# Optimization experiments

Measured on AMD Instinct MI355X. Metric: run time of the kernel, lower is better.

## Reference

```python
import jax, jax.numpy as jnp
import numpy as np

B, T, D, N, K, H = 2, 2048, 2048, 16, 8, 128
WINDOW = 1024
SOFT_CAP = 50.0
Q_SCALE = H ** -0.5  # query_pre_attn_scalar
ROPE_BASE = 10000
ROPE_SCALE = 1.0
K_MASK = -2.3819763e38


def apply_rope(x, positions, base_frequency=ROPE_BASE, scale_factor=ROPE_SCALE):
    # x: [B, T, n, H], positions: [B, T]
    head_dim = x.shape[-1]
    fraction = 2.0 * jnp.arange(head_dim // 2, dtype=jnp.float32) / head_dim
    timescale = base_frequency ** fraction  # [H/2]
    sin_inp = positions[..., None].astype(jnp.float32) / timescale  # [B,T,H/2]
    sin_inp = sin_inp[..., None, :] / scale_factor  # [B,T,1,H/2]
    sin, cos = jnp.sin(sin_inp), jnp.cos(sin_inp)
    x1, x2 = jnp.split(x, 2, axis=-1)
    out = jnp.concatenate([x1 * cos - x2 * sin, x2 * cos + x1 * sin], axis=-1)
    return out.astype(x.dtype)


def rms_norm(x, scale, eps=1e-6):
    var = jnp.mean(jnp.square(x.astype(jnp.float32)), axis=-1, keepdims=True)
    normed = x * jax.lax.rsqrt(var + eps)
    return (normed * (1.0 + scale)).astype(x.dtype)


def setup_inputs() -> dict:
    key = jax.random.key(0)
    ks = jax.random.split(key, 4)
    x = jax.random.normal(ks[0], (B, T, D), jnp.float32)
    segment_pos = jnp.tile(jnp.arange(T, dtype=jnp.int32)[None, :], (B, 1))
    attn_mask = jnp.tril(jnp.ones((T, T), dtype=bool))[None].repeat(B, axis=0)
    w_q = jax.random.normal(ks[1], (N, D, H), jnp.float32) * (D ** -0.5)
    w_kv = jax.random.normal(ks[2], (2, K, D, H), jnp.float32) * (D ** -0.5)
    w_o = jax.random.normal(ks[3], (N, H, D), jnp.float32) * ((N * H) ** -0.5)
    q_norm_scale = jnp.zeros((H,), jnp.float32)
    k_norm_scale = jnp.zeros((H,), jnp.float32)
    return dict(x=x, w_q=w_q, w_kv=w_kv, w_o=w_o,
                q_norm_scale=q_norm_scale, k_norm_scale=k_norm_scale,
                segment_pos=segment_pos, attn_mask=attn_mask)


def reference(x, w_q, w_kv, w_o, q_norm_scale, k_norm_scale, segment_pos, attn_mask):
    # projections
    q = jnp.einsum('BTD,NDH->BTNH', x, w_q)              # [B,T,N,H]
    kv = jnp.einsum('BSD,CKDH->CBSKH', x, w_kv)          # [2,B,S,K,H]
    k, v = kv[0], kv[1]
    # QK RMSNorm
    q = rms_norm(q, q_norm_scale)
    k = rms_norm(k, k_norm_scale)
    # RoPE + query scaling
    q = apply_rope(q, segment_pos) * Q_SCALE
    k = apply_rope(k, segment_pos)
    # GQA logits
    G = N // K
    qg = q.reshape(B, T, K, G, H)
    logits = jnp.einsum('BTKGH,BSKH->BTKGS', qg, k).reshape(B, T, N, T)
    # soft cap
    logits = jnp.tanh(logits / SOFT_CAP) * SOFT_CAP
    # sliding-window mask combined with causal attn_mask
    pos_q = segment_pos[:, :, None]
    pos_k = segment_pos[:, None, :]
    sliding = (pos_k > pos_q - WINDOW) & (pos_k < pos_q + WINDOW)
    mask = attn_mask & sliding                           # [B,T,S]
    padded = jnp.where(mask[:, :, None, :], logits, K_MASK)
    probs = jax.nn.softmax(padded, axis=-1).astype(k.dtype)
    # GQA weighted values
    enc = jnp.einsum('BTKGS,BSKH->BTKGH', probs.reshape(B, T, K, G, T), v)
    enc = enc.reshape(B, T, N, H)
    # split/concat of navigator vs scribe heads is an identity on output
    return jnp.einsum('BTNH,NHD->BTD', enc, w_o)
```

## Files before the change

### kernel.cpp

```cpp
#include <hip/hip_runtime.h>
#include <stdint.h>

typedef __attribute__((ext_vector_type(8))) short short8;
typedef __attribute__((ext_vector_type(4))) float f32x4;

#define B_ 2
#define T_ 2048
#define D_ 2048
#define N_ 16
#define KH_ 8
#define H_ 128
#define WINDOW_ 1024

__device__ __forceinline__ uint16_t f2bf(float f) {
  union { float f; uint32_t u; } a; a.f = f;
  uint32_t u = a.u;
  return (uint16_t)((u + 0x7FFFu + ((u >> 16) & 1u)) >> 16);
}

__device__ __forceinline__ void gl_lds16(const void* g, void* l) {
  __builtin_amdgcn_global_load_lds((const __attribute__((address_space(1))) void*)g,
                                   (__attribute__((address_space(3))) void*)l, 16, 0, 0);
}

__global__ __launch_bounds__(256) void k_f2b4(const float* __restrict__ src,
                                              uint16_t* __restrict__ dst, long n) {
  long i = ((long)blockIdx.x * 256 + threadIdx.x) * 4;
  if (i >= n) return;
  float4 v = *(const float4*)(src + i);
  uint64_t p = (uint64_t)f2bf(v.x) | ((uint64_t)f2bf(v.y) << 16) |
               ((uint64_t)f2bf(v.z) << 32) | ((uint64_t)f2bf(v.w) << 48);
  *(uint64_t*)(dst + i) = p;
}

__global__ __launch_bounds__(256)
void k_transpose_f2b(const float* __restrict__ src, uint16_t* __restrict__ dst,
                     int R, int C, int nb1, long sbs1, long sbs2, long dbs,
                     long src_off, int srs) {
  __shared__ float tile[32][33];
  int z = blockIdx.z;
  int b1 = z % nb1, b2 = z / nb1;
  const float* s = src + src_off + (long)b1 * sbs1 + (long)b2 * sbs2;
  uint16_t* d = dst + (long)z * dbs;
  int c0 = blockIdx.x * 32, r0 = blockIdx.y * 32;
  int x = threadIdx.x, y = threadIdx.y;
#pragma unroll
  for (int j = 0; j < 4; ++j)
    tile[y + j * 8][x] = s[(long)(r0 + y + j * 8) * srs + (c0 + x)];
  __syncthreads();
#pragma unroll
  for (int j = 0; j < 4; ++j)
    d[(long)(c0 + y + j * 8) * R + (r0 + x)] = f2bf(tile[x][y + j * 8]);
}

__global__ __launch_bounds__(256)
void k_transpose_v(const float* __restrict__ kvg, uint16_t* __restrict__ vbt) {
  __shared__ float tile[32][33];
  int z = blockIdx.z;
  int kh = z % KH_, b = z / KH_;
  const float* s = kvg + (long)b * T_ * 2048 + 1024 + kh * H_;
  uint16_t* d = vbt + (long)z * H_ * T_;
  int h0 = blockIdx.x * 32, s0 = blockIdx.y * 32;
  int x = threadIdx.x, y = threadIdx.y;
#pragma unroll
  for (int j = 0; j < 4; ++j)
    tile[y + j * 8][x] = s[(long)(s0 + y + j * 8) * 2048 + (h0 + x)];
  __syncthreads();
#pragma unroll
  for (int j = 0; j < 4; ++j) {
    int h = h0 + y + j * 8;
    int si = s0 + x;
    int ss = (si & ~63) | ((((si >> 3) & 7) ^ (h & 7)) << 3) | (si & 7);
    d[(long)h * T_ + ss] = f2bf(tile[x][y + j * 8]);
  }
}

__global__ __launch_bounds__(512, 2)
void k_gemm8(const uint16_t* __restrict__ A, const uint16_t* __restrict__ Bt,
             float* __restrict__ C0, float* __restrict__ C1, int nbx, int splitc) {
  __shared__ __align__(16) uint16_t Ls[2][2][2][128 * 64];
  int tid = threadIdx.x, lane = tid & 63, w = tid >> 6;
  int wm = w >> 2, wn = w & 3;
  int fr = lane & 15, fgrp = lane >> 4;
  int bid = blockIdx.x;
  int k2 = bid >> 3;
  long by = (bid & 7) * 2 + k2 / nbx;
  long bx = k2 % nbx;
  long row0 = by * 256, col0 = bx * 256;

  int trow = tid >> 3;
  int kse = (((tid & 7) * 16) ^ ((trow & 7) << 4)) >> 1;
  const uint16_t* aS[2] = { A + (row0 + trow) * 2048 + kse,
                            A + (row0 + 128 + trow) * 2048 + kse };
  const uint16_t* bS[2] = { Bt + (col0 + trow) * 2048 + kse,
                            Bt + (col0 + 128 + trow) * 2048 + kse };
  char* ldsbase = (char*)Ls + w * 1024;

  int kx[2] = { (fgrp * 16) ^ ((fr & 7) << 4), (64 + fgrp * 16) ^ ((fr & 7) << 4) };
  int aoffb = (wm * 64 + fr) * 128;
  int boffb = (wn * 32 + fr) * 128;
  const char* LA = (const char*)Ls;
  const char* LB = LA + 65536;

  f32x4 acc[2][2][4][2];
#pragma unroll
  for (int qm = 0; qm < 2; ++qm)
#pragma unroll
    for (int qn = 0; qn < 2; ++qn)
#pragma unroll
      for (int m = 0; m < 4; ++m)
#pragma unroll
        for (int n = 0; n < 2; ++n) acc[qm][qn][m][n] = (f32x4){0.f, 0.f, 0.f, 0.f};

#define STG(MAT, SLOT, HALF, KT) do {                                      \
    const uint16_t* _g = (MAT ? bS[HALF] : aS[HALF]) + (KT) * 64;          \
    char* _l = ldsbase + (MAT) * 65536 + (SLOT) * 32768 + (HALF) * 16384;  \
    gl_lds16(_g, _l);                                                      \
    gl_lds16(_g + 64 * 2048, _l + 8192);                                   \
  } while (0)

#define PH(SLOT, QM, QN, STMT, VM) do {                                               \
    short8 _a[4][2], _b[2][2];                                                        \
    _Pragma("unroll") for (int m = 0; m < 4; ++m) {                                   \
      _a[m][0] = *(const short8*)(LA + (SLOT)*32768 + (QM)*16384 + aoffb + m*2048 + kx[0]); \
      _a[m][1] = *(const short8*)(LA + (SLOT)*32768 + (QM)*16384 + aoffb + m*2048 + kx[1]); } \
    _Pragma("unroll") for (int n = 0; n < 2; ++n) {                                   \
      _b[n][0] = *(const short8*)(LB + (SLOT)*32768 + (QN)*16384 + boffb + n*2048 + kx[0]); \
      _b[n][1] = *(const short8*)(LB + (SLOT)*32768 + (QN)*16384 + boffb + n*2048 + kx[1]); } \
    STMT;                                                                             \
    __builtin_amdgcn_s_barrier();                                                     \
    asm volatile("s_waitcnt lgkmcnt(0)" ::: "memory");                                \
    __builtin_amdgcn_sched_barrier(0);                                                \
    __builtin_amdgcn_s_setprio(1);                                                    \
    _Pragma("unroll") for (int m = 0; m < 4; ++m)                                     \
      _Pragma("unroll") for (int n = 0; n < 2; ++n) {                                 \
        acc[QM][QN][m][n] = __builtin_amdgcn_mfma_f32_16x16x32_bf16(_a[m][0], _b[n][0], acc[QM][QN][m][n], 0, 0, 0); \
        acc[QM][QN][m][n] = __builtin_amdgcn_mfma_f32_16x16x32_bf16(_a[m][1], _b[n][1], acc[QM][QN][m][n], 0, 0, 0); } \
    __builtin_amdgcn_s_setprio(0);                                                    \
    if (VM) { asm volatile("s_waitcnt vmcnt(4)" ::: "memory");                        \
              __builtin_amdgcn_sched_barrier(0); }                                    \
    __builtin_amdgcn_s_barrier();                                                     \
    __builtin_amdgcn_sched_barrier(0);                                                \
  } while (0)

  STG(0, 0, 0, 0); STG(1, 0, 0, 0); STG(1, 0, 1, 0); STG(0, 0, 1, 0);
  STG(0, 1, 0, 1); STG(1, 1, 0, 1);
  asm volatile("s_waitcnt vmcnt(4)" ::: "memory");
  __builtin_amdgcn_sched_barrier(0);
  __builtin_amdgcn_s_barrier();

#pragma unroll 1
  for (int it = 0; it < 16; ++it) {
    int t1 = 2 * it + 1, t2 = (2 * it + 2) & 31, t3 = (2 * it + 3) & 31;
    PH(0, 0, 0, STG(1, 1, 1, t1), 0);
    PH(0, 0, 1, STG(0, 1, 1, t1), 0);
    PH(0, 1, 0, STG(0, 0, 0, t2), 0);
    PH(0, 1, 1, STG(1, 0, 0, t2), 1);
    PH(1, 0, 0, STG(1, 0, 1, t2), 0);
    PH(1, 0, 1, STG(0, 0, 1, t2), 0);
    PH(1, 1, 0, STG(0, 1, 0, t3), 0);
    PH(1, 1, 1, STG(1, 1, 0, t3), 1);
  }
#undef PH
#undef STG

  int og = fgrp * 4;
  bool hic = (col0 >= splitc);
  float* Cb = hic ? C1 : C0;
  long cb = col0 - (hic ? splitc : 0);
#pragma unroll
  for (int qm = 0; qm < 2; ++qm)
#pragma unroll
    for (int qn = 0; qn < 2; ++qn)
#pragma unroll
      for (int m = 0; m < 4; ++m)
#pragma unroll
        for (int n = 0; n < 2; ++n) {
          long r = row0 + qm * 128 + wm * 64 + m * 16 + og;
          long c = cb + qn * 128 + wn * 32 + n * 16 + fr;
          float* cp = Cb + r * 2048 + c;
#pragma unroll
          for (int i = 0; i < 4; ++i) cp[(long)i * 2048] = acc[qm][qn][m][n][i];
        }
}

__global__ __launch_bounds__(512, 2)
void k_gemm8n(const uint16_t* __restrict__ A, const uint16_t* __restrict__ Bt,
              float* __restrict__ C, int nbx) {
  __shared__ __align__(16) uint16_t LsA[2][2][128 * 64];
  __shared__ __align__(16) uint16_t LsB[2][128 * 64];
  int tid = threadIdx.x, lane = tid & 63, w = tid >> 6;
  int wm = w >> 2, wn = w & 3;
  int fr = lane & 15, fgrp = lane >> 4;
  int bid = blockIdx.x;
  int k2 = bid >> 3;
  long by = (bid & 7) * 2 + k2 / nbx;
  long bx = k2 % nbx;
  long row0 = by * 256, col0 = bx * 128;

  int trow = tid >> 3;
  int kse = (((tid & 7) * 16) ^ ((trow & 7) << 4)) >> 1;
  const uint16_t* aS[2] = { A + (row0 + trow) * 2048 + kse,
                            A + (row0 + 128 + trow) * 2048 + kse };
  const uint16_t* bS = Bt + (col0 + trow) * 2048 + kse;
  char* ldsA_w = (char*)LsA + w * 1024;
  char* ldsB_w = (char*)LsB + w * 1024;

  int kx[2] = { (fgrp * 16) ^ ((fr & 7) << 4), (64 + fgrp * 16) ^ ((fr & 7) << 4) };
  int aoffb = (wm * 64 + fr) * 128;
  int boffb = (wn * 32 + fr) * 128;
  const char* LA = (const char*)LsA;
  const char* LB = (const char*)LsB;

  f32x4 acc[2][4][2];
#pragma unroll
  for (int qm = 0; qm < 2; ++qm)
#pragma unroll
    for (int m = 0; m < 4; ++m)
#pragma unroll
      for (int n = 0; n < 2; ++n) acc[qm][m][n] = (f32x4){0.f, 0.f, 0.f, 0.f};

#define STGA(SLOT, HALF, KT) do {                                \
    const uint16_t* _g = aS[HALF] + (KT) * 64;                   \
    char* _l = ldsA_w + (SLOT) * 32768 + (HALF) * 16384;         \
    gl_lds16(_g, _l);                                            \
    gl_lds16(_g + 64 * 2048, _l + 8192);                         \
  } while (0)
#define STGB(SLOT, KT) do {                                      \
    const uint16_t* _g = bS + (KT) * 64;                         \
    char* _l = ldsB_w + (SLOT) * 16384;                          \
    gl_lds16(_g, _l);                                            \
    gl_lds16(_g + 64 * 2048, _l + 8192);                         \
  } while (0)

#define PHN(SLOT, QM, STMT, VM) do {                                                  \
    short8 _a[4][2], _b[2][2];                                                        \
    _Pragma("unroll") for (int m = 0; m < 4; ++m) {                                   \
      _a[m][0] = *(const short8*)(LA + (SLOT)*32768 + (QM)*16384 + aoffb + m*2048 + kx[0]); \
      _a[m][1] = *(const short8*)(LA + (SLOT)*32768 + (QM)*16384 + aoffb + m*2048 + kx[1]); } \
    _Pragma("unroll") for (int n = 0; n < 2; ++n) {                                   \
      _b[n][0] = *(const short8*)(LB + (SLOT)*16384 + boffb + n*2048 + kx[0]);        \
      _b[n][1] = *(const short8*)(LB + (SLOT)*16384 + boffb + n*2048 + kx[1]); }      \
    STMT;                                                                             \
    __builtin_amdgcn_s_barrier();                                                     \
    asm volatile("s_waitcnt lgkmcnt(0)" ::: "memory");                                \
    __builtin_amdgcn_sched_barrier(0);                                                \
    __builtin_amdgcn_s_setprio(1);                                                    \
    _Pragma("unroll") for (int m = 0; m < 4; ++m)                                     \
      _Pragma("unroll") for (int n = 0; n < 2; ++n) {                                 \
        acc[QM][m][n] = __builtin_amdgcn_mfma_f32_16x16x32_bf16(_a[m][0], _b[n][0], acc[QM][m][n], 0, 0, 0); \
        acc[QM][m][n] = __builtin_amdgcn_mfma_f32_16x16x32_bf16(_a[m][1], _b[n][1], acc[QM][m][n], 0, 0, 0); } \
    __builtin_amdgcn_s_setprio(0);                                                    \
    if (VM) { asm volatile("s_waitcnt vmcnt(2)" ::: "memory");                        \
              __builtin_amdgcn_sched_barrier(0); }                                    \
    __builtin_amdgcn_s_barrier();                                                     \
    __builtin_amdgcn_sched_barrier(0);                                                \
  } while (0)

  STGA(0, 0, 0); STGA(0, 1, 0); STGB(0, 0); STGA(1, 0, 1);
  asm volatile("s_waitcnt vmcnt(2)" ::: "memory");
  __builtin_amdgcn_sched_barrier(0);
  __builtin_amdgcn_s_barrier();

#pragma unroll 1
  for (int it = 0; it < 16; ++it) {
    int t1 = 2 * it + 1, t2 = (2 * it + 2) & 31, t3 = (2 * it + 3) & 31;
    PHN(0, 0, { STGA(1, 1, t1); STGB(1, t1); }, 0);
    PHN(0, 1, STGA(0, 0, t2), 1);
    PHN(1, 0, { STGA(0, 1, t2); STGB(0, t2); }, 0);
    PHN(1, 1, STGA(1, 0, t3), 1);
  }
#undef PHN
#undef STGA
#undef STGB

  int og = fgrp * 4;
#pragma unroll
  for (int qm = 0; qm < 2; ++qm)
#pragma unroll
    for (int m = 0; m < 4; ++m)
#pragma unroll
      for (int n = 0; n < 2; ++n) {
        long r = row0 + qm * 128 + wm * 64 + m * 16 + og;
        long c = col0 + wn * 32 + n * 16 + fr;
        float* cp = C + r * 2048 + c;
#pragma unroll
        for (int i = 0; i < 4; ++i) cp[(long)i * 2048] = acc[qm][m][n][i];
      }
}

__global__ __launch_bounds__(256)
void k_qpost(const float* __restrict__ qg, const float* __restrict__ qs,
             uint16_t* __restrict__ qb) {
  int gw = blockIdx.x * 4 + (threadIdx.x >> 6);
  int lane = threadIdx.x & 63;
  int bt = gw / N_;
  int t = bt % T_;
  const float* src = qg + (long)gw * H_;
  float x1 = src[lane], x2 = src[lane + 64];
  float ssq = x1 * x1 + x2 * x2;
#pragma unroll
  for (int off = 1; off < 64; off <<= 1) ssq += __shfl_xor(ssq, off);
  float inv = rsqrtf(ssq * (1.0f / 128.0f) + 1e-6f);
  float n1 = x1 * inv * (1.0f + qs[lane]);
  float n2 = x2 * inv * (1.0f + qs[lane + 64]);
  float ts = powf(10000.0f, (float)lane * (2.0f / 128.0f));
  float ang = (float)t / ts;
  float sn, cs;
  sincosf(ang, &sn, &cs);
  const float QSC = 0.08838834764831845f;
  uint16_t* dp = qb + (long)gw * H_;
  dp[lane] = f2bf((n1 * cs - n2 * sn) * QSC);
  dp[lane + 64] = f2bf((n2 * cs + n1 * sn) * QSC);
}

__global__ __launch_bounds__(256)
void k_kpost(const float* __restrict__ kvg, const float* __restrict__ ks,
             uint16_t* __restrict__ kb) {
  int gw = blockIdx.x * 4 + (threadIdx.x >> 6);
  int lane = threadIdx.x & 63;
  int kh = gw % KH_;
  int bt = gw / KH_;
  int t = bt % T_, b = bt / T_;
  const float* src = kvg + (long)bt * (KH_ * H_ * 2) + kh * H_;
  float x1 = src[lane], x2 = src[lane + 64];
  float ssq = x1 * x1 + x2 * x2;
#pragma unroll
  for (int off = 1; off < 64; off <<= 1) ssq += __shfl_xor(ssq, off);
  float inv = rsqrtf(ssq * (1.0f / 128.0f) + 1e-6f);
  float n1 = x1 * inv * (1.0f + ks[lane]);
  float n2 = x2 * inv * (1.0f + ks[lane + 64]);
  float ts = powf(10000.0f, (float)lane * (2.0f / 128.0f));
  float ang = (float)t / ts;
  float sn, cs;
  sincosf(ang, &sn, &cs);
  int sw = (t & 7) << 3;
  uint16_t* dp = kb + ((long)(b * KH_ + kh) * T_ + t) * H_;
  dp[lane ^ sw] = f2bf(n1 * cs - n2 * sn);
  dp[(lane + 64) ^ sw] = f2bf(n2 * cs + n1 * sn);
}

__global__ __launch_bounds__(256, 4)
void k_attn(const uint16_t* __restrict__ qb, const uint16_t* __restrict__ kb,
            const uint16_t* __restrict__ vbt, uint16_t* __restrict__ enc) {
  __shared__ uint16_t Ks[64 * 128];
  __shared__ uint16_t Vs[128 * 64];
  __shared__ uint16_t Pl[4][16 * 64];
  int tid = threadIdx.x, lane = tid & 63, w = tid >> 6;
  int nt = T_ / 64;
  int blk = blockIdx.x;
  int tq = nt - 1 - (blk >> 5);
  int bn = blk & 31;
  int n = bn % N_, b = bn / N_;
  int kh = n >> 1;
  int t0 = tq * 64;
  int tw = t0 + w * 16;
  int fr = lane & 15, fgrp = lane >> 4, fk = fgrp * 8;
  int sw3 = fr & 7;

  const uint16_t* qrow = qb + ((long)(b * T_ + tw + fr) * N_ + n) * H_;
  short8 aq[4];
#pragma unroll
  for (int kk = 0; kk < 4; ++kk) aq[kk] = *(const short8*)(qrow + kk * 32 + fk);

  float lrow[4];
  f32x4 o[8];
#pragma unroll
  for (int i = 0; i < 4; ++i) lrow[i] = 0.0f;
#pragma unroll
  for (int hf = 0; hf < 8; ++hf) o[hf] = (f32x4){0.f, 0.f, 0.f, 0.f};

  int s_begin = t0 - (WINDOW_ - 1);
  if (s_begin < 0) s_begin = 0;
  s_begin &= ~63;
  int s_endex = t0 + 64;

  const uint16_t* kbase = kb + (long)(b * KH_ + kh) * T_ * H_;
  const uint16_t* vbase = vbt + (long)(b * KH_ + kh) * H_ * T_;
  int krow_st = tid >> 4, kcol_st = (tid & 15) * 8;
  int vrow_st = tid >> 3, vcol_st = (tid & 7) * 8;
  char* ldsK = (char*)Ks + w * 1024;
  char* ldsV = (char*)Vs + w * 1024;
  uint16_t* Pw = Pl[w];

  for (int s0 = s_begin; s0 < s_endex; s0 += 64) {
    __syncthreads();
#pragma unroll
    for (int j = 0; j < 4; ++j) {
      gl_lds16(kbase + (long)(s0 + j * 16 + krow_st) * H_ + kcol_st, ldsK + j * 4096);
      gl_lds16(vbase + (long)(j * 32 + vrow_st) * T_ + s0 + vcol_st, ldsV + j * 4096);
    }
    __syncthreads();
    if (s0 > tw + 15 || s0 + 63 < tw - (WINDOW_ - 1)) continue;

    f32x4 sc[4];
#pragma unroll
    for (int kc = 0; kc < 4; ++kc) {
      f32x4 a = (f32x4){0.f, 0.f, 0.f, 0.f};
      const uint16_t* kr = Ks + (kc * 16 + fr) * 128;
#pragma unroll
      for (int kk = 0; kk < 4; ++kk) {
        short8 bk = *(const short8*)(kr + ((((kk << 2) | fgrp) ^ sw3) << 3));
        a = __builtin_amdgcn_mfma_f32_16x16x32_bf16(aq[kk], bk, a, 0, 0, 0);
      }
      sc[kc] = a;
    }

    bool full = (s0 + 63 <= tw) && (s0 >= tw + 16 - WINDOW_);
#define SMBODY(FULL)                                                              \
    _Pragma("unroll") for (int i = 0; i < 4; ++i) {                               \
      int r = fgrp * 4 + i;                                                       \
      int rsw = (r & 7) << 3;                                                     \
      int trowq = tw + r;                                                         \
      float ps = 0.f;                                                             \
      _Pragma("unroll") for (int kc = 0; kc < 4; ++kc) {                          \
        float v = sc[kc][i];                                                      \
        float xx = v * 0.02f;                                                     \
        xx = fminf(1.0f, fmaxf(-1.0f, xx));                                       \
        float u = xx * xx;                                                        \
        float tt = xx * fmaf(u, fmaf(u, fmaf(u, -0.053968254f, 0.13333334f),      \
                                     -0.33333334f), 1.0f);                        \
        float p = __expf(fmaf(tt, 50.0f, -20.0f));                                \
        if (!(FULL)) {                                                            \
          int s = s0 + kc * 16 + fr;                                              \
          bool ok = (s <= trowq) && (s > trowq - WINDOW_);                        \
          p = ok ? p : 0.0f;                                                      \
        }                                                                         \
        ps += p;                                                                  \
        Pw[r * 64 + ((kc * 16 + fr) ^ rsw)] = f2bf(p);                            \
      }                                                                           \
      lrow[i] += ps;                                                              \
    }
    if (full) { SMBODY(true) } else { SMBODY(false) }
#undef SMBODY

    short8 pa0 = *(const short8*)(Pw + fr * 64 + ((fgrp ^ sw3) << 3));
    short8 pa1 = *(const short8*)(Pw + fr * 64 + (((4 | fgrp) ^ sw3) << 3));
#pragma unroll
    for (int hf = 0; hf < 8; ++hf) {
      const uint16_t* vr = Vs + (hf * 16 + fr) * 64;
      short8 bv0 = *(const short8*)(vr + ((fgrp ^ sw3) << 3));
      short8 bv1 = *(const short8*)(vr + (((4 | fgrp) ^ sw3) << 3));
      o[hf] = __builtin_amdgcn_mfma_f32_16x16x32_bf16(pa0, bv0, o[hf], 0, 0, 0);
      o[hf] = __builtin_amdgcn_mfma_f32_16x16x32_bf16(pa1, bv1, o[hf], 0, 0, 0);
    }
  }

#pragma unroll
  for (int i = 0; i < 4; ++i) {
#pragma unroll
    for (int off = 1; off < 16; off <<= 1) lrow[i] += __shfl_xor(lrow[i], off);
    lrow[i] = 1.0f / lrow[i];
  }
#pragma unroll
  for (int hf = 0; hf < 8; ++hf)
#pragma unroll
    for (int i = 0; i < 4; ++i) {
      int t = tw + fgrp * 4 + i;
      float val = o[hf][i] * lrow[i];
      enc[((long)(b * T_ + t) * N_ + n) * H_ + hf * 16 + fr] = f2bf(val);
    }
}

extern "C" void kernel_launch(void* const* d_in, const int* in_sizes, int n_in,
                              void* d_out, int out_size, void* d_ws, size_t ws_size,
                              hipStream_t stream) {
  const float* x = (const float*)d_in[0];
  const float* w_q = (const float*)d_in[1];
  const float* w_kv = (const float*)d_in[2];
  const float* w_o = (const float*)d_in[3];
  const float* qns = (const float*)d_in[4];
  const float* kns = (const float*)d_in[5];
  float* out = (float*)d_out;

  uint16_t* ws = (uint16_t*)d_ws;
  uint16_t* xb    = ws;
  uint16_t* wq_t  = xb    + 8388608;
  uint16_t* wkv_t = wq_t  + 4194304;
  uint16_t* wo_t  = wkv_t + 4194304;
  uint16_t* qb    = wo_t  + 4194304;
  uint16_t* kb    = qb    + 8388608;
  uint16_t* vbt   = kb    + 4194304;
  uint16_t* enc   = vbt   + 4194304;
  float* kvg = (float*)(enc + 8388608);
  if (ws_size < (size_t)125829120) return;

  dim3 tb(32, 8);
  k_f2b4<<<8192, 256, 0, stream>>>(x, xb, 8388608);
  k_transpose_f2b<<<dim3(4, 64, 16), tb, 0, stream>>>(w_q, wq_t, 2048, 128, 16,
      (long)D_ * H_, 0, (long)H_ * D_, 0, H_);
  k_transpose_f2b<<<dim3(4, 64, 8), tb, 0, stream>>>(w_kv, wkv_t, 2048, 128, 8,
      (long)D_ * H_, 0, (long)H_ * D_, 0, H_);
  k_transpose_f2b<<<dim3(4, 64, 8), tb, 0, stream>>>(w_kv, wkv_t + 1024 * 2048, 2048, 128, 8,
      (long)D_ * H_, 0, (long)H_ * D_, (long)KH_ * D_ * H_, H_);
  k_transpose_f2b<<<dim3(64, 64, 1), tb, 0, stream>>>(w_o, wo_t, 2048, 2048, 1,
      0, 0, 0, 0, 2048);
  k_gemm8<<<256, 512, 0, stream>>>(xb, wq_t, out, kvg, 16, 2048);
  k_qpost<<<(B_ * T_ * N_) / 4, 256, 0, stream>>>(out, qns, qb);
  k_kpost<<<(B_ * T_ * KH_) / 4, 256, 0, stream>>>(kvg, kns, kb);
  k_transpose_v<<<dim3(4, 64, 16), tb, 0, stream>>>(kvg, vbt);
  k_attn<<<B_ * N_ * (T_ / 64), 256, 0, stream>>>(qb, kb, vbt, enc);
  k_gemm8n<<<256, 512, 0, stream>>>(enc, wo_t, out, 16);
}
```

Measured before the change: 234.5 us.

## Reuse LDS fragments across GEMM phases and deepen global prefetch pipeline

The GEMM main loop now keeps A and B fragments in persistent registers and reorders the four quadrant phases (00, 01, 11, 10) so each phase reloads only the operand that changed, cutting LDS reads per k-tile. The global-to-LDS staging schedule is reworked so both halves of the next k-tile are prefetched up front, with the vmcnt waits raised from 4 to 8 to allow more loads in flight. This trades extra VGPR pressure from the held B fragments for less LDS traffic. The new slot/stage ordering must still respect the buffer-reuse hazards.

Measured after the change: 228.5 us. 1.03x faster.

```diff
diff --git a/kernel.cpp b/kernel.cpp
--- a/kernel.cpp
+++ b/kernel.cpp
@@ -112,6 +112,9 @@
 #pragma unroll
         for (int n = 0; n < 2; ++n) acc[qm][qn][m][n] = (f32x4){0.f, 0.f, 0.f, 0.f};
 
+  short8 RA[4][2];
+  short8 RB[2][2][2];
+
 #define STG(MAT, SLOT, HALF, KT) do {                                      \
     const uint16_t* _g = (MAT ? bS[HALF] : aS[HALF]) + (KT) * 64;          \
     char* _l = ldsbase + (MAT) * 65536 + (SLOT) * 32768 + (HALF) * 16384;  \
@@ -119,49 +122,57 @@
     gl_lds16(_g + 64 * 2048, _l + 8192);                                   \
   } while (0)
 
-#define PH(SLOT, QM, QN, STMT, VM) do {                                               \
-    short8 _a[4][2], _b[2][2];                                                        \
-    _Pragma("unroll") for (int m = 0; m < 4; ++m) {                                   \
-      _a[m][0] = *(const short8*)(LA + (SLOT)*32768 + (QM)*16384 + aoffb + m*2048 + kx[0]); \
-      _a[m][1] = *(const short8*)(LA + (SLOT)*32768 + (QM)*16384 + aoffb + m*2048 + kx[1]); } \
-    _Pragma("unroll") for (int n = 0; n < 2; ++n) {                                   \
-      _b[n][0] = *(const short8*)(LB + (SLOT)*32768 + (QN)*16384 + boffb + n*2048 + kx[0]); \
-      _b[n][1] = *(const short8*)(LB + (SLOT)*32768 + (QN)*16384 + boffb + n*2048 + kx[1]); } \
-    STMT;                                                                             \
+#define RDA(SLOT, QM) do {                                                             \
+    _Pragma("unroll") for (int m = 0; m < 4; ++m) {                                    \
+      RA[m][0] = *(const short8*)(LA + (SLOT)*32768 + (QM)*16384 + aoffb + m*2048 + kx[0]); \
+      RA[m][1] = *(const short8*)(LA + (SLOT)*32768 + (QM)*16384 + aoffb + m*2048 + kx[1]); } \
+  } while (0)
+
+#define RDB(SLOT, QN) do {                                                             \
+    _Pragma("unroll") for (int n = 0; n < 2; ++n) {                                    \
+      RB[QN][n][0] = *(const short8*)(LB + (SLOT)*32768 + (QN)*16384 + boffb + n*2048 + kx[0]); \
+      RB[QN][n][1] = *(const short8*)(LB + (SLOT)*32768 + (QN)*16384 + boffb + n*2048 + kx[1]); } \
+  } while (0)
+
+#define PHX(RDSTMT, STGSTMT, QM, QN, VM) do {                                         \
+    RDSTMT;                                                                           \
+    STGSTMT;                                                                          \
     __builtin_amdgcn_s_barrier();                                                     \
     asm volatile("s_waitcnt lgkmcnt(0)" ::: "memory");                                \
     __builtin_amdgcn_sched_barrier(0);                                                \
     __builtin_amdgcn_s_setprio(1);                                                    \
     _Pragma("unroll") for (int m = 0; m < 4; ++m)                                     \
       _Pragma("unroll") for (int n = 0; n < 2; ++n) {                                 \
-        acc[QM][QN][m][n] = __builtin_amdgcn_mfma_f32_16x16x32_bf16(_a[m][0], _b[n][0], acc[QM][QN][m][n], 0, 0, 0); \
-        acc[QM][QN][m][n] = __builtin_amdgcn_mfma_f32_16x16x32_bf16(_a[m][1], _b[n][1], acc[QM][QN][m][n], 0, 0, 0); } \
+        acc[QM][QN][m][n] = __builtin_amdgcn_mfma_f32_16x16x32_bf16(RA[m][0], RB[QN][n][0], acc[QM][QN][m][n], 0, 0, 0); \
+        acc[QM][QN][m][n] = __builtin_amdgcn_mfma_f32_16x16x32_bf16(RA[m][1], RB[QN][n][1], acc[QM][QN][m][n], 0, 0, 0); } \
     __builtin_amdgcn_s_setprio(0);                                                    \
-    if (VM) { asm volatile("s_waitcnt vmcnt(4)" ::: "memory");                        \
+    if (VM) { asm volatile("s_waitcnt vmcnt(8)" ::: "memory");                        \
               __builtin_amdgcn_sched_barrier(0); }                                    \
     __builtin_amdgcn_s_barrier();                                                     \
     __builtin_amdgcn_sched_barrier(0);                                                \
   } while (0)
 
   STG(0, 0, 0, 0); STG(1, 0, 0, 0); STG(1, 0, 1, 0); STG(0, 0, 1, 0);
-  STG(0, 1, 0, 1); STG(1, 1, 0, 1);
-  asm volatile("s_waitcnt vmcnt(4)" ::: "memory");
+  STG(0, 1, 0, 1); STG(1, 1, 0, 1); STG(1, 1, 1, 1); STG(0, 1, 1, 1);
+  asm volatile("s_waitcnt vmcnt(8)" ::: "memory");
   __builtin_amdgcn_sched_barrier(0);
   __builtin_amdgcn_s_barrier();
 
 #pragma unroll 1
   for (int it = 0; it < 16; ++it) {
-    int t1 = 2 * it + 1, t2 = (2 * it + 2) & 31, t3 = (2 * it + 3) & 31;
-    PH(0, 0, 0, STG(1, 1, 1, t1), 0);
-    PH(0, 0, 1, STG(0, 1, 1, t1), 0);
-    PH(0, 1, 0, STG(0, 0, 0, t2), 0);
-    PH(0, 1, 1, STG(1, 0, 0, t2), 1);
-    PH(1, 0, 0, STG(1, 0, 1, t2), 0);
-    PH(1, 0, 1, STG(0, 0, 1, t2), 0);
-    PH(1, 1, 0, STG(0, 1, 0, t3), 0);
-    PH(1, 1, 1, STG(1, 1, 0, t3), 1);
+    int t2 = (2 * it + 2) & 31, t3 = (2 * it + 3) & 31;
+    PHX({ RDA(0, 0); RDB(0, 0); }, {}, 0, 0, 0);
+    PHX({ RDB(0, 1); }, { STG(0, 0, 0, t2); STG(1, 0, 0, t2); }, 0, 1, 0);
+    PHX({ RDA(0, 1); }, { STG(1, 0, 1, t2); }, 1, 1, 0);
+    PHX({}, { STG(0, 0, 1, t2); }, 1, 0, 1);
+    PHX({ RDA(1, 0); RDB(1, 0); }, {}, 0, 0, 0);
+    PHX({ RDB(1, 1); }, { STG(0, 1, 0, t3); STG(1, 1, 0, t3); }, 0, 1, 0);
+    PHX({ RDA(1, 1); }, { STG(1, 1, 1, t3); }, 1, 1, 0);
+    PHX({}, { STG(0, 1, 1, t3); }, 1, 0, 1);
   }
-#undef PH
+#undef PHX
+#undef RDA
+#undef RDB
 #undef STG
 
   int og = fgrp * 4;
```
